# Performance work log

Measured on AMD Instinct MI355X. Metric: run time of the kernel, lower is better.

Reference implementation:

```python
import jax, jax.numpy as jnp
import numpy as np

B, L, D, H = 2, 2048, 1024, 16
HD = D // H
SCALE = HD ** (-0.5)


def setup_inputs() -> dict:
    key = jax.random.key(0)
    ks = jax.random.split(key, 12)
    mk = lambda k, shape: (0.02 * jax.random.normal(k, shape, dtype=jnp.float32))
    return {
        "x_real": jax.random.normal(ks[0], (B, L, D), dtype=jnp.float32),
        "x_imag": jax.random.normal(ks[1], (B, L, D), dtype=jnp.float32),
        "wq_r": mk(ks[2], (D, D)),
        "wq_i": mk(ks[3], (D, D)),
        "wk_r": mk(ks[4], (D, D)),
        "wk_i": mk(ks[5], (D, D)),
        "wv_r": mk(ks[6], (D, D)),
        "wv_i": mk(ks[7], (D, D)),
        "wo_r": mk(ks[8], (D, D)),
        "wo_i": mk(ks[9], (D, D)),
        "bo_r": jnp.zeros((D,), dtype=jnp.float32),
        "bo_i": jnp.zeros((D,), dtype=jnp.float32),
    }


def _clinear(xr, xi, wr, wi):
    # (a+bi)(c+di): real = a@Wr^T - b@Wi^T ; imag = a@Wi^T + b@Wr^T
    r = xr @ wr.T - xi @ wi.T
    i = xr @ wi.T + xi @ wr.T
    return r, i


def _heads(t):
    # [B,L,D] -> [B,H,L,hd]
    return t.reshape(B, L, H, HD).transpose(0, 2, 1, 3)


def reference(x_real, x_imag, wq_r, wq_i, wk_r, wk_i, wv_r, wv_i, wo_r, wo_i, bo_r, bo_i):
    Qr, Qi = _clinear(x_real, x_imag, wq_r, wq_i)
    Kr, Ki = _clinear(x_real, x_imag, wk_r, wk_i)
    Vr, Vi = _clinear(x_real, x_imag, wv_r, wv_i)
    Qr, Qi, Kr, Ki, Vr, Vi = map(_heads, (Qr, Qi, Kr, Ki, Vr, Vi))

    # real part of complex dot product: Re(Q)Re(K)^T + Im(Q)Im(K)^T
    scores = (jnp.einsum("bhqd,bhkd->bhqk", Qr, Kr)
              + jnp.einsum("bhqd,bhkd->bhqk", Qi, Ki)) * SCALE
    causal = jnp.tril(jnp.ones((L, L), dtype=bool))
    scores = jnp.where(causal, scores, -jnp.inf)
    w = jax.nn.softmax(scores, axis=-1)

    out_r = jnp.einsum("bhqk,bhkd->bhqd", w, Vr)
    out_i = jnp.einsum("bhqk,bhkd->bhqd", w, Vi)
    merge = lambda t: t.transpose(0, 2, 1, 3).reshape(B, L, D)
    out_r, out_i = merge(out_r), merge(out_i)

    yr, yi = _clinear(out_r, out_i, wo_r, wo_i)
    return yr + bo_r, yi + bo_i
```

## Files before the change

### kernel.cpp

```cpp
#include <hip/hip_runtime.h>
#include <hip/hip_bf16.h>


using f32x4  = __attribute__((ext_vector_type(4))) float;
using short8 = __attribute__((ext_vector_type(8))) short;
using bf16_t = __hip_bfloat16;

#define AS1 __attribute__((address_space(1)))
#define AS3 __attribute__((address_space(3)))

__device__ __forceinline__ void gload_lds16(const bf16_t* g, bf16_t* l) {
  __builtin_amdgcn_global_load_lds((const AS1 unsigned int*)g, (AS3 unsigned int*)l, 16, 0, 0);
}

__device__ __forceinline__ unsigned short bfbits(float f) {
  union { bf16_t h; unsigned short u; } c; c.h = __float2bfloat16(f); return c.u;
}

__global__ void pack_x_k(const float* __restrict__ xr, const float* __restrict__ xi,
                         bf16_t* __restrict__ out) {
  const int total4 = 4096 * 2048 / 4;
  for (int idx = blockIdx.x * blockDim.x + threadIdx.x; idx < total4;
       idx += gridDim.x * blockDim.x) {
    int m = idx >> 9, k = (idx & 511) * 4;
    const float* src = (k < 1024) ? (xr + (size_t)m * 1024 + k)
                                  : (xi + (size_t)m * 1024 + (k - 1024));
    float4 v = *(const float4*)src;
    unsigned int lo = (unsigned)bfbits(v.x) | ((unsigned)bfbits(v.y) << 16);
    unsigned int hi = (unsigned)bfbits(v.z) | ((unsigned)bfbits(v.w) << 16);
    *(uint2*)(out + (size_t)idx * 4) = make_uint2(lo, hi);
  }
}

__global__ void pack_wqkv_k(const float* __restrict__ wqr, const float* __restrict__ wqi,
                            const float* __restrict__ wkr, const float* __restrict__ wki,
                            const float* __restrict__ wvr, const float* __restrict__ wvi,
                            bf16_t* __restrict__ out) {
  const int total4 = 6144 * 2048 / 4;
  for (int idx = blockIdx.x * blockDim.x + threadIdx.x; idx < total4;
       idx += gridDim.x * blockDim.x) {
    int row = idx >> 9, k = (idx & 511) * 4;
    int sec = row >> 10, r1 = row & 1023;
    bool lowk = (k < 1024);
    int kk = lowk ? k : (k - 1024);
    const float* base = wqr; float sg = 1.f;
    switch (sec) {
      case 0: base = lowk ? wqr : wqi; sg = lowk ? 1.f : -1.f; break;
      case 1: base = lowk ? wqi : wqr; break;
      case 2: base = lowk ? wkr : wki; sg = lowk ? 1.f : -1.f; break;
      case 3: base = lowk ? wki : wkr; break;
      case 4: base = lowk ? wvr : wvi; sg = lowk ? 1.f : -1.f; break;
      case 5: base = lowk ? wvi : wvr; break;
    }
    float4 v = *(const float4*)(base + (size_t)r1 * 1024 + kk);
    unsigned int lo = (unsigned)bfbits(v.x * sg) | ((unsigned)bfbits(v.y * sg) << 16);
    unsigned int hi = (unsigned)bfbits(v.z * sg) | ((unsigned)bfbits(v.w * sg) << 16);
    *(uint2*)(out + (size_t)idx * 4) = make_uint2(lo, hi);
  }
}

__global__ void pack_wo_k(const float* __restrict__ wor, const float* __restrict__ woi,
                          bf16_t* __restrict__ out) {
  const int total4 = 2048 * 2048 / 4;
  for (int idx = blockIdx.x * blockDim.x + threadIdx.x; idx < total4;
       idx += gridDim.x * blockDim.x) {
    int row = idx >> 9, k = (idx & 511) * 4;
    int sec = row >> 10, r1 = row & 1023;
    bool lowk = (k < 1024);
    int kk = lowk ? k : (k - 1024);
    const float* base; float sg = 1.f;
    if (sec == 0) { base = lowk ? wor : woi; sg = lowk ? 1.f : -1.f; }
    else          { base = lowk ? woi : wor; }
    float4 v = *(const float4*)(base + (size_t)r1 * 1024 + kk);
    unsigned int lo = (unsigned)bfbits(v.x * sg) | ((unsigned)bfbits(v.y * sg) << 16);
    unsigned int hi = (unsigned)bfbits(v.z * sg) | ((unsigned)bfbits(v.w * sg) << 16);
    *(uint2*)(out + (size_t)idx * 4) = make_uint2(lo, hi);
  }
}

__device__ __forceinline__ void gemm_core(const bf16_t* __restrict__ A,
                                          const bf16_t* __restrict__ W,
                                          int m0, int n0, f32x4 (&acc)[4][4]) {
  __shared__ __align__(16) bf16_t sA[128 * 64];
  __shared__ __align__(16) bf16_t sB[128 * 64];
  const int tid = threadIdx.x;
  const int lane = tid & 63, w = tid >> 6;
  const int wr = w >> 1, wc = w & 1;
  const int quad = lane >> 4, m16 = lane & 15;
  const int srow = w * 32 + (lane >> 3);
  const int gcol = (((lane & 7) ^ (lane >> 3)) * 8);
  const int swz7 = m16 & 7;
  for (int k0 = 0; k0 < 2048; k0 += 64) {
    __syncthreads();
#pragma unroll
    for (int i = 0; i < 4; ++i) {
      gload_lds16(A + (size_t)(m0 + srow + i * 8) * 2048 + k0 + gcol,
                  sA + (size_t)(w * 32 + i * 8) * 64 + lane * 8);
      gload_lds16(W + (size_t)(n0 + srow + i * 8) * 2048 + k0 + gcol,
                  sB + (size_t)(w * 32 + i * 8) * 64 + lane * 8);
    }
    __syncthreads();
#pragma unroll
    for (int kk = 0; kk < 2; ++kk) {
      short8 af[4], bf[4];
#pragma unroll
      for (int i = 0; i < 4; ++i)
        af[i] = *(const short8*)(sA + (wr * 64 + i * 16 + m16) * 64 +
                                 ((kk * 4 + quad) ^ swz7) * 8);
#pragma unroll
      for (int j = 0; j < 4; ++j)
        bf[j] = *(const short8*)(sB + (wc * 64 + j * 16 + m16) * 64 +
                                 ((kk * 4 + quad) ^ swz7) * 8);
#pragma unroll
      for (int i = 0; i < 4; ++i)
#pragma unroll
        for (int j = 0; j < 4; ++j)
          acc[i][j] = __builtin_amdgcn_mfma_f32_16x16x32_bf16(af[i], bf[j], acc[i][j], 0, 0, 0);
    }
  }
}

__global__ __launch_bounds__(512, 2) void gemm_qkv_k(const bf16_t* __restrict__ A,
                                                     const bf16_t* __restrict__ W,
                                                     bf16_t* __restrict__ qk,
                                                     bf16_t* __restrict__ vt) {
  __shared__ __align__(16) bf16_t sA[2][256 * 64];
  __shared__ __align__(16) bf16_t sB[2][192 * 64];
  const int tid = threadIdx.x, lane = tid & 63, w = tid >> 6;
  const int wm = w >> 2, wn = w & 3;
  const int quad = lane >> 4, m16 = lane & 15;
  const int swz7 = m16 & 7;
  const int m0 = blockIdx.x * 256, n0 = blockIdx.y * 192;
  const int NT = 32;

  const int l3 = lane >> 3;
  const int gcol = (((lane & 7) ^ l3) * 8);

  f32x4 acc[8][3] = {};

  auto stageA = [&](int buf, int half, int k0) {
#pragma unroll
    for (int i = 0; i < 2; ++i)
      gload_lds16(A + (size_t)(m0 + half * 128 + w * 16 + i * 8 + l3) * 2048 + k0 + gcol,
                  &sA[buf][(size_t)(half * 128 + w * 16 + i * 8) * 64] + lane * 8);
  };
  auto stageB = [&](int buf, int c, int k0) {
    gload_lds16(W + (size_t)(n0 + c * 64 + w * 8 + l3) * 2048 + k0 + gcol,
                &sB[buf][(size_t)(c * 64 + w * 8) * 64] + lane * 8);
  };
  auto rdA = [&](const bf16_t* sAx, int mf, int kk) -> short8 {
    return *(const short8*)(sAx + (wm * 128 + mf * 16 + m16) * 64 +
                            ((kk * 4 + quad) ^ swz7) * 8);
  };
  auto rdB = [&](const bf16_t* sBx, int j, int kk) -> short8 {
    return *(const short8*)(sBx + (wn * 48 + j * 16 + m16) * 64 +
                            ((kk * 4 + quad) ^ swz7) * 8);
  };

  stageA(0, 0, 0); stageA(0, 1, 0);
  stageB(0, 0, 0); stageB(0, 1, 0); stageB(0, 2, 0);
  stageA(1, 0, 64); stageA(1, 1, 64);
  stageB(1, 0, 64); stageB(1, 1, 64); stageB(1, 2, 64);
  asm volatile("s_waitcnt vmcnt(7)" ::: "memory");
  __builtin_amdgcn_s_barrier();

  short8 A0[4], A1[4], B0[3], B1[3];
#pragma unroll
  for (int i = 0; i < 4; ++i) A0[i] = rdA(sA[0], i, 0);
#pragma unroll
  for (int j = 0; j < 3; ++j) B0[j] = rdB(sB[0], j, 0);

  for (int t = 0; t < NT; ++t) {
    const int p = t & 1, q = p ^ 1;
    const bf16_t* sAp = sA[p];
    const bf16_t* sBp = sB[p];
    const bf16_t* sAq = sA[q];
    const bf16_t* sBq = sB[q];
    const bool stg = (t + 1 < NT);

#pragma unroll
    for (int i = 0; i < 4; ++i) A1[i] = rdA(sAp, 4 + i, 0);
    if (stg) stageA(q, 0, (t + 1) * 64);
    __builtin_amdgcn_s_setprio(1);
#pragma unroll
    for (int i = 0; i < 4; ++i)
#pragma unroll
      for (int j = 0; j < 3; ++j)
        acc[i][j] = __builtin_amdgcn_mfma_f32_16x16x32_bf16(A0[i], B0[j], acc[i][j], 0, 0, 0);
    __builtin_amdgcn_s_setprio(0);

#pragma unroll
    for (int i = 0; i < 4; ++i) A0[i] = rdA(sAp, i, 1);
#pragma unroll
    for (int j = 0; j < 3; ++j) B1[j] = rdB(sBp, j, 1);
    if (stg) stageA(q, 1, (t + 1) * 64);
    __builtin_amdgcn_s_setprio(1);
#pragma unroll
    for (int i = 0; i < 4; ++i)
#pragma unroll
      for (int j = 0; j < 3; ++j)
        acc[4 + i][j] = __builtin_amdgcn_mfma_f32_16x16x32_bf16(A1[i], B0[j], acc[4 + i][j], 0, 0, 0);
    __builtin_amdgcn_s_setprio(0);

#pragma unroll
    for (int i = 0; i < 4; ++i) A1[i] = rdA(sAp, 4 + i, 1);
    __builtin_amdgcn_s_setprio(1);
#pragma unroll
    for (int i = 0; i < 4; ++i)
#pragma unroll
      for (int j = 0; j < 3; ++j)
        acc[i][j] = __builtin_amdgcn_mfma_f32_16x16x32_bf16(A0[i], B1[j], acc[i][j], 0, 0, 0);
    __builtin_amdgcn_s_setprio(0);

    asm volatile("s_waitcnt vmcnt(0)" ::: "memory");
    __builtin_amdgcn_s_barrier();

    if (stg) {
#pragma unroll
      for (int i = 0; i < 4; ++i) A0[i] = rdA(sAq, i, 0);
#pragma unroll
      for (int j = 0; j < 3; ++j) B0[j] = rdB(sBq, j, 0);
    }
    if (t + 2 < NT) {
      stageB(p, 0, (t + 2) * 64); stageB(p, 1, (t + 2) * 64); stageB(p, 2, (t + 2) * 64);
    }
    __builtin_amdgcn_s_setprio(1);
#pragma unroll
    for (int i = 0; i < 4; ++i)
#pragma unroll
      for (int j = 0; j < 3; ++j)
        acc[4 + i][j] = __builtin_amdgcn_mfma_f32_16x16x32_bf16(A1[i], B1[j], acc[4 + i][j], 0, 0, 0);
    __builtin_amdgcn_s_setprio(0);
  }

#pragma unroll
  for (int mf = 0; mf < 8; ++mf) {
    const int rowb = m0 + wm * 128 + mf * 16 + quad * 4;
#pragma unroll
    for (int nf = 0; nf < 3; ++nf) {
      const int col = n0 + wn * 48 + nf * 16 + m16;
      if (col < 4096) {
        const float sc = (col < 2048) ? 0.125f : 1.f;
#pragma unroll
        for (int r = 0; r < 4; ++r)
          qk[(size_t)(rowb + r) * 4096 + col] = __float2bfloat16(acc[mf][nf][r] * sc);
      } else {
        const int vcol = col - 4096;
        const int ri = vcol >> 10, dfeat = vcol & 1023;
        const int b = rowb >> 11, seq = rowb & 2047;
        const size_t vrow = (size_t)(b * 2048 + (dfeat >> 6) * 128 + ri * 64 + (dfeat & 63));
        unsigned int lo = (unsigned)bfbits(acc[mf][nf][0]) | ((unsigned)bfbits(acc[mf][nf][1]) << 16);
        unsigned int hi = (unsigned)bfbits(acc[mf][nf][2]) | ((unsigned)bfbits(acc[mf][nf][3]) << 16);
        *(uint2*)(vt + vrow * 2048 + seq) = make_uint2(lo, hi);
      }
    }
  }
}

__global__ __launch_bounds__(256) void gemm_out_k(const bf16_t* __restrict__ A,
                                                  const bf16_t* __restrict__ W,
                                                  const float* __restrict__ bor,
                                                  const float* __restrict__ boi,
                                                  float* __restrict__ out) {
  f32x4 acc[4][4] = {};
  const int m0 = blockIdx.x * 128, n0 = blockIdx.y * 128;
  gemm_core(A, W, m0, n0, acc);
  const int lane = threadIdx.x & 63, w = threadIdx.x >> 6;
  const int wr = w >> 1, wc = w & 1, quad = lane >> 4, m16 = lane & 15;
#pragma unroll
  for (int i = 0; i < 4; ++i) {
    const int rowb = m0 + wr * 64 + i * 16 + quad * 4;
#pragma unroll
    for (int j = 0; j < 4; ++j) {
      const int col = n0 + wc * 64 + j * 16 + m16;
      float bias; float* op;
      if (col < 1024) { bias = bor[col]; op = out + col; }
      else            { bias = boi[col - 1024]; op = out + 4194304 + (col - 1024); }
#pragma unroll
      for (int r = 0; r < 4; ++r)
        op[(size_t)(rowb + r) * 1024] = acc[i][j][r] + bias;
    }
  }
}

__global__ __launch_bounds__(512, 4) void attn_k(const bf16_t* __restrict__ qk,
                                                 const bf16_t* __restrict__ vt,
                                                 bf16_t* __restrict__ acat) {
  __shared__ __align__(16) bf16_t sK[64 * 128];
  __shared__ __align__(16) bf16_t sV[144 * 64];
  __shared__ __align__(16) bf16_t sP[8][16 * 72];
  const int tid = threadIdx.x, lane = tid & 63, w = tid >> 6;
  const int wq = w & 3, sub = w >> 2;
  const int quad = lane >> 4, m16 = lane & 15;
  const int x = blockIdx.x, bh = blockIdx.y, b = bh >> 4, h = bh & 15;
  const size_t qkrow0 = (size_t)b * 2048;
  const int qA = x * 64, qB = (31 - x) * 64;
  const int nT = 32 - x;
  const int swz7 = m16 & 7;
  const int qbase = (sub ? qB : qA) + wq * 16;

  if (tid < 256) {
    const int rr = tid >> 4, cb = (tid & 15) * 4;
    const bf16_t v = __float2bfloat16(rr == 0 ? 1.f : 0.f);
#pragma unroll
    for (int i = 0; i < 4; ++i) sV[(128 + rr) * 64 + cb + i] = v;
  }

  short8 qf[4];
  {
    const bf16_t* qa = qk + (qkrow0 + qbase + m16) * 4096;
#pragma unroll
    for (int kk = 0; kk < 4; ++kk) {
      const int col = (kk >> 1) * 1024 + h * 64 + (kk & 1) * 32 + quad * 8;
      qf[kk] = *(const short8*)(qa + col);
    }
  }
  f32x4 o[9];
#pragma unroll
  for (int j = 0; j < 9; ++j) o[j] = (f32x4){0.f, 0.f, 0.f, 0.f};

  const int qrow = qbase + quad * 4;

  const int kl4 = lane >> 4, kl15 = lane & 15;
  const int vl3 = lane >> 3;
  const int vg7 = ((lane & 7) ^ vl3) * 8;

  for (int t = 0; t < nT; ++t) {
    const int k0 = t * 64;
    __syncthreads();
#pragma unroll
    for (int i = 0; i < 2; ++i) {
      const int row = w * 8 + i * 4 + kl4;
      const int g = kl15 ^ (row & 7);
      const int col = 2048 + (g >> 3) * 1024 + h * 64 + (g & 7) * 8;
      gload_lds16(qk + (qkrow0 + k0 + row) * 4096 + col,
                  sK + (size_t)(w * 8 + i * 4) * 128 + lane * 8);
    }
#pragma unroll
    for (int i = 0; i < 2; ++i) {
      const int row = w * 16 + i * 8 + vl3;
      gload_lds16(vt + ((size_t)bh * 128 + row) * 2048 + k0 + vg7,
                  sV + (size_t)(w * 16 + i * 8) * 64 + lane * 8);
    }
    __syncthreads();

    const bool act = sub ? true : (t <= x);
    if (act) {
      const bool dg = sub ? (t == nT - 1) : (t == x);

      f32x4 sv[4];
#pragma unroll
      for (int jt = 0; jt < 4; ++jt) {
        f32x4 a = (f32x4){0.f, 0.f, 0.f, 0.f};
#pragma unroll
        for (int kk = 0; kk < 4; ++kk) {
          short8 kf = *(const short8*)(sK + (jt * 16 + m16) * 128 +
                                       ((kk * 4 + quad) ^ swz7) * 8);
          a = __builtin_amdgcn_mfma_f32_16x16x32_bf16(qf[kk], kf, a, 0, 0, 0);
        }
        sv[jt] = a;
      }

      bf16_t* pw = sP[w];
#pragma unroll
      for (int jt = 0; jt < 4; ++jt)
#pragma unroll
        for (int r = 0; r < 4; ++r) {
          float s = sv[jt][r];
          if (dg && (k0 + jt * 16 + m16 > qrow + r)) s = -1e30f;
          pw[(quad * 4 + r) * 72 + jt * 16 + m16] = __float2bfloat16(__expf(s));
        }
      asm volatile("s_waitcnt lgkmcnt(0)" ::: "memory");

#pragma unroll
      for (int kc = 0; kc < 2; ++kc) {
        short8 p = *(const short8*)(pw + m16 * 72 + kc * 32 + quad * 8);
#pragma unroll
        for (int j = 0; j < 9; ++j) {
          short8 vf = *(const short8*)(sV + (j * 16 + m16) * 64 +
                                       ((kc * 4 + quad) ^ swz7) * 8);
          o[j] = __builtin_amdgcn_mfma_f32_16x16x32_bf16(p, vf, o[j], 0, 0, 0);
        }
      }
    }
  }

  float inv[4];
#pragma unroll
  for (int r = 0; r < 4; ++r)
    inv[r] = 1.f / __shfl(o[8][r], lane & 48);
#pragma unroll
  for (int j = 0; j < 8; ++j) {
    const int d = j * 16 + m16;
    const int col = (d < 64) ? (h * 64 + d) : (1024 + h * 64 + (d - 64));
#pragma unroll
    for (int r = 0; r < 4; ++r)
      acat[((size_t)b * 2048 + qrow + r) * 2048 + col] = __float2bfloat16(o[j][r] * inv[r]);
  }
}

extern "C" void kernel_launch(void* const* d_in, const int* in_sizes, int n_in,
                              void* d_out, int out_size, void* d_ws, size_t ws_size,
                              hipStream_t stream) {
  const float* xr  = (const float*)d_in[0];
  const float* xi  = (const float*)d_in[1];
  const float* wqr = (const float*)d_in[2];
  const float* wqi = (const float*)d_in[3];
  const float* wkr = (const float*)d_in[4];
  const float* wki = (const float*)d_in[5];
  const float* wvr = (const float*)d_in[6];
  const float* wvi = (const float*)d_in[7];
  const float* wor = (const float*)d_in[8];
  const float* woi = (const float*)d_in[9];
  const float* bor = (const float*)d_in[10];
  const float* boi = (const float*)d_in[11];
  float* out = (float*)d_out;

  char* ws = (char*)d_ws;
  bf16_t* Xcat = (bf16_t*)(ws);
  bf16_t* Wqkv = (bf16_t*)(ws + 16777216ull);
  bf16_t* QKb  = (bf16_t*)(ws + 41943040ull);
  bf16_t* Vt   = (bf16_t*)(ws + 75497472ull);
  bf16_t* Acat = (bf16_t*)(ws + 92274688ull);
  bf16_t* Wo   = (bf16_t*)(ws + 109051904ull);

  pack_x_k<<<2048, 256, 0, stream>>>(xr, xi, Xcat);
  pack_wqkv_k<<<2048, 256, 0, stream>>>(wqr, wqi, wkr, wki, wvr, wvi, Wqkv);
  pack_wo_k<<<1024, 256, 0, stream>>>(wor, woi, Wo);
  gemm_qkv_k<<<dim3(16, 32), 512, 0, stream>>>(Xcat, Wqkv, QKb, Vt);
  attn_k<<<dim3(16, 32), 512, 0, stream>>>(QKb, Vt, Acat);
  gemm_out_k<<<dim3(32, 16), 256, 0, stream>>>(Acat, Wo, bor, boi, out);
}
```

Measured before the change: 352.3 us.

## Pipeline output GEMM with double-buffered LDS and rebalance QKV staging and attention order

Replaces the single-buffered output projection GEMM with a 512-thread, 128x256-tile kernel that double-buffers LDS and interleaves MFMA groups with register-prefetched fragments, mirroring the QKV GEMM design. This aims to hide global-to-LDS load latency that the old per-iteration sync-load-compute loop exposed. In the QKV GEMM, A tiles are now staged two iterations ahead together with B instead of one ahead mid-loop. The attention kernel also interleaves block indices so that heavy and light causal blocks alternate. Larger tiles reduce the output GEMM grid to 256 blocks, which may leave some compute units underused.

```diff
diff --git a/kernel.cpp b/kernel.cpp
--- a/kernel.cpp
+++ b/kernel.cpp
@@ -78,48 +78,6 @@
   }
 }
 
-__device__ __forceinline__ void gemm_core(const bf16_t* __restrict__ A,
-                                          const bf16_t* __restrict__ W,
-                                          int m0, int n0, f32x4 (&acc)[4][4]) {
-  __shared__ __align__(16) bf16_t sA[128 * 64];
-  __shared__ __align__(16) bf16_t sB[128 * 64];
-  const int tid = threadIdx.x;
-  const int lane = tid & 63, w = tid >> 6;
-  const int wr = w >> 1, wc = w & 1;
-  const int quad = lane >> 4, m16 = lane & 15;
-  const int srow = w * 32 + (lane >> 3);
-  const int gcol = (((lane & 7) ^ (lane >> 3)) * 8);
-  const int swz7 = m16 & 7;
-  for (int k0 = 0; k0 < 2048; k0 += 64) {
-    __syncthreads();
-#pragma unroll
-    for (int i = 0; i < 4; ++i) {
-      gload_lds16(A + (size_t)(m0 + srow + i * 8) * 2048 + k0 + gcol,
-                  sA + (size_t)(w * 32 + i * 8) * 64 + lane * 8);
-      gload_lds16(W + (size_t)(n0 + srow + i * 8) * 2048 + k0 + gcol,
-                  sB + (size_t)(w * 32 + i * 8) * 64 + lane * 8);
-    }
-    __syncthreads();
-#pragma unroll
-    for (int kk = 0; kk < 2; ++kk) {
-      short8 af[4], bf[4];
-#pragma unroll
-      for (int i = 0; i < 4; ++i)
-        af[i] = *(const short8*)(sA + (wr * 64 + i * 16 + m16) * 64 +
-                                 ((kk * 4 + quad) ^ swz7) * 8);
-#pragma unroll
-      for (int j = 0; j < 4; ++j)
-        bf[j] = *(const short8*)(sB + (wc * 64 + j * 16 + m16) * 64 +
-                                 ((kk * 4 + quad) ^ swz7) * 8);
-#pragma unroll
-      for (int i = 0; i < 4; ++i)
-#pragma unroll
-        for (int j = 0; j < 4; ++j)
-          acc[i][j] = __builtin_amdgcn_mfma_f32_16x16x32_bf16(af[i], bf[j], acc[i][j], 0, 0, 0);
-    }
-  }
-}
-
 __global__ __launch_bounds__(512, 2) void gemm_qkv_k(const bf16_t* __restrict__ A,
                                                      const bf16_t* __restrict__ W,
                                                      bf16_t* __restrict__ qk,
@@ -177,10 +135,10 @@
     const bf16_t* sAq = sA[q];
     const bf16_t* sBq = sB[q];
     const bool stg = (t + 1 < NT);
+    const bool stg2 = (t + 2 < NT);
 
 #pragma unroll
     for (int i = 0; i < 4; ++i) A1[i] = rdA(sAp, 4 + i, 0);
-    if (stg) stageA(q, 0, (t + 1) * 64);
     __builtin_amdgcn_s_setprio(1);
 #pragma unroll
     for (int i = 0; i < 4; ++i)
@@ -193,7 +151,6 @@
     for (int i = 0; i < 4; ++i) A0[i] = rdA(sAp, i, 1);
 #pragma unroll
     for (int j = 0; j < 3; ++j) B1[j] = rdB(sBp, j, 1);
-    if (stg) stageA(q, 1, (t + 1) * 64);
     __builtin_amdgcn_s_setprio(1);
 #pragma unroll
     for (int i = 0; i < 4; ++i)
@@ -221,7 +178,8 @@
 #pragma unroll
       for (int j = 0; j < 3; ++j) B0[j] = rdB(sBq, j, 0);
     }
-    if (t + 2 < NT) {
+    if (stg2) {
+      stageA(p, 0, (t + 2) * 64); stageA(p, 1, (t + 2) * 64);
       stageB(p, 0, (t + 2) * 64); stageB(p, 1, (t + 2) * 64); stageB(p, 2, (t + 2) * 64);
     }
     __builtin_amdgcn_s_setprio(1);
@@ -257,28 +215,134 @@
   }
 }
 
-__global__ __launch_bounds__(256) void gemm_out_k(const bf16_t* __restrict__ A,
-                                                  const bf16_t* __restrict__ W,
-                                                  const float* __restrict__ bor,
-                                                  const float* __restrict__ boi,
-                                                  float* __restrict__ out) {
+__global__ __launch_bounds__(512, 2) void gemm_out_k(const bf16_t* __restrict__ A,
+                                                     const bf16_t* __restrict__ W,
+                                                     const float* __restrict__ bor,
+                                                     const float* __restrict__ boi,
+                                                     float* __restrict__ out) {
+  __shared__ __align__(16) bf16_t sA[2][128 * 64];
+  __shared__ __align__(16) bf16_t sB[2][256 * 64];
+  const int tid = threadIdx.x, lane = tid & 63, w = tid >> 6;
+  const int wm = w >> 2, wn = w & 3;
+  const int quad = lane >> 4, m16 = lane & 15;
+  const int swz7 = m16 & 7;
+  const int m0 = blockIdx.x * 128, n0 = blockIdx.y * 256;
+  const int NT = 32;
+
+  const int l3 = lane >> 3;
+  const int gcol = (((lane & 7) ^ l3) * 8);
+
   f32x4 acc[4][4] = {};
-  const int m0 = blockIdx.x * 128, n0 = blockIdx.y * 128;
-  gemm_core(A, W, m0, n0, acc);
-  const int lane = threadIdx.x & 63, w = threadIdx.x >> 6;
-  const int wr = w >> 1, wc = w & 1, quad = lane >> 4, m16 = lane & 15;
-#pragma unroll
-  for (int i = 0; i < 4; ++i) {
-    const int rowb = m0 + wr * 64 + i * 16 + quad * 4;
-#pragma unroll
-    for (int j = 0; j < 4; ++j) {
-      const int col = n0 + wc * 64 + j * 16 + m16;
+
+  auto stageA = [&](int buf, int k0) {
+#pragma unroll
+    for (int i = 0; i < 2; ++i)
+      gload_lds16(A + (size_t)(m0 + w * 16 + i * 8 + l3) * 2048 + k0 + gcol,
+                  &sA[buf][(size_t)(w * 16 + i * 8) * 64] + lane * 8);
+  };
+  auto stageB = [&](int buf, int half, int k0) {
+#pragma unroll
+    for (int i = 0; i < 2; ++i)
+      gload_lds16(W + (size_t)(n0 + half * 128 + w * 16 + i * 8 + l3) * 2048 + k0 + gcol,
+                  &sB[buf][(size_t)(half * 128 + w * 16 + i * 8) * 64] + lane * 8);
+  };
+  auto rdA = [&](const bf16_t* sAx, int mf, int kk) -> short8 {
+    return *(const short8*)(sAx + (wm * 64 + mf * 16 + m16) * 64 +
+                            ((kk * 4 + quad) ^ swz7) * 8);
+  };
+  auto rdB = [&](const bf16_t* sBx, int nf, int kk) -> short8 {
+    return *(const short8*)(sBx + (wn * 64 + nf * 16 + m16) * 64 +
+                            ((kk * 4 + quad) ^ swz7) * 8);
+  };
+
+  stageA(0, 0);
+  stageB(0, 0, 0); stageB(0, 1, 0);
+  stageA(1, 64);
+  stageB(1, 0, 64); stageB(1, 1, 64);
+  asm volatile("s_waitcnt vmcnt(6)" ::: "memory");
+  __builtin_amdgcn_s_barrier();
+
+  short8 A0[2], A1[2], B0[4], B1[4];
+#pragma unroll
+  for (int i = 0; i < 2; ++i) A0[i] = rdA(sA[0], i, 0);
+#pragma unroll
+  for (int j = 0; j < 4; ++j) B0[j] = rdB(sB[0], j, 0);
+
+  for (int t = 0; t < NT; ++t) {
+    const int p = t & 1, q = p ^ 1;
+    const bf16_t* sAp = sA[p];
+    const bf16_t* sBp = sB[p];
+    const bf16_t* sAq = sA[q];
+    const bf16_t* sBq = sB[q];
+    const bool stg = (t + 1 < NT);
+    const bool stg2 = (t + 2 < NT);
+
+#pragma unroll
+    for (int i = 0; i < 2; ++i) A1[i] = rdA(sAp, 2 + i, 0);
+    __builtin_amdgcn_s_setprio(1);
+#pragma unroll
+    for (int i = 0; i < 2; ++i)
+#pragma unroll
+      for (int j = 0; j < 4; ++j)
+        acc[i][j] = __builtin_amdgcn_mfma_f32_16x16x32_bf16(A0[i], B0[j], acc[i][j], 0, 0, 0);
+    __builtin_amdgcn_s_setprio(0);
+
+#pragma unroll
+    for (int i = 0; i < 2; ++i) A0[i] = rdA(sAp, i, 1);
+#pragma unroll
+    for (int j = 0; j < 4; ++j) B1[j] = rdB(sBp, j, 1);
+    __builtin_amdgcn_s_setprio(1);
+#pragma unroll
+    for (int i = 0; i < 2; ++i)
+#pragma unroll
+      for (int j = 0; j < 4; ++j)
+        acc[2 + i][j] = __builtin_amdgcn_mfma_f32_16x16x32_bf16(A1[i], B0[j], acc[2 + i][j], 0, 0, 0);
+    __builtin_amdgcn_s_setprio(0);
+
+#pragma unroll
+    for (int i = 0; i < 2; ++i) A1[i] = rdA(sAp, 2 + i, 1);
+    __builtin_amdgcn_s_setprio(1);
+#pragma unroll
+    for (int i = 0; i < 2; ++i)
+#pragma unroll
+      for (int j = 0; j < 4; ++j)
+        acc[i][j] = __builtin_amdgcn_mfma_f32_16x16x32_bf16(A0[i], B1[j], acc[i][j], 0, 0, 0);
+    __builtin_amdgcn_s_setprio(0);
+
+    asm volatile("s_waitcnt vmcnt(0)" ::: "memory");
+    __builtin_amdgcn_s_barrier();
+
+    if (stg) {
+#pragma unroll
+      for (int i = 0; i < 2; ++i) A0[i] = rdA(sAq, i, 0);
+#pragma unroll
+      for (int j = 0; j < 4; ++j) B0[j] = rdB(sBq, j, 0);
+    }
+    if (stg2) {
+      stageA(p, (t + 2) * 64);
+      stageB(p, 0, (t + 2) * 64); stageB(p, 1, (t + 2) * 64);
+    }
+    __builtin_amdgcn_s_setprio(1);
+#pragma unroll
+    for (int i = 0; i < 2; ++i)
+#pragma unroll
+      for (int j = 0; j < 4; ++j)
+        acc[2 + i][j] = __builtin_amdgcn_mfma_f32_16x16x32_bf16(A1[i], B1[j], acc[2 + i][j], 0, 0, 0);
+    __builtin_amdgcn_s_setprio(0);
+  }
+
+#pragma unroll
+  for (int mf = 0; mf < 4; ++mf) {
+    const int rowb = m0 + wm * 64 + mf * 16 + quad * 4;
+#pragma unroll
+    for (int nf = 0; nf < 4; ++nf) {
+      const int col = n0 + wn * 64 + nf * 16 + m16;
       float bias; float* op;
       if (col < 1024) { bias = bor[col]; op = out + col; }
       else            { bias = boi[col - 1024]; op = out + 4194304 + (col - 1024); }
 #pragma unroll
       for (int r = 0; r < 4; ++r)
-        op[(size_t)(rowb + r) * 1024] = acc[i][j][r] + bias;
+        op[(size_t)(rowb + r) * 1024] = acc[mf][nf][r] + bias;
     }
   }
 }
@@ -292,7 +356,9 @@
   const int tid = threadIdx.x, lane = tid & 63, w = tid >> 6;
   const int wq = w & 3, sub = w >> 2;
   const int quad = lane >> 4, m16 = lane & 15;
-  const int x = blockIdx.x, bh = blockIdx.y, b = bh >> 4, h = bh & 15;
+  const int bx = blockIdx.x;
+  const int x = (bx & 1) ? (15 - (bx >> 1)) : (bx >> 1);
+  const int bh = blockIdx.y, b = bh >> 4, h = bh & 15;
   const size_t qkrow0 = (size_t)b * 2048;
   const int qA = x * 64, qB = (31 - x) * 64;
   const int nT = 32 - x;
@@ -429,5 +495,5 @@
   pack_wo_k<<<1024, 256, 0, stream>>>(wor, woi, Wo);
   gemm_qkv_k<<<dim3(16, 32), 512, 0, stream>>>(Xcat, Wqkv, QKb, Vt);
   attn_k<<<dim3(16, 32), 512, 0, stream>>>(QKb, Vt, Acat);
-  gemm_out_k<<<dim3(32, 16), 256, 0, stream>>>(Acat, Wo, bor, boi, out);
-}
+  gemm_out_k<<<dim3(32, 8), 512, 0, stream>>>(Acat, Wo, bor, boi, out);
+}
```

After: 338.8 us. 1.04x faster.
